# Performance work log

Measured on AMD Instinct MI355X. Metric: run time of the kernel, lower is better.

## Reference

```python
import jax, jax.numpy as jnp
import numpy as np
import math

# Model dims (match init_kwargs)
N = 2048      # columns
DS = 64       # d_state
DI = 256      # d_input
DV = 64       # d_vote
K = 512       # k_active = int(N * 0.25)
H = 4         # bus attention heads
HD = DV // H  # head dim
MULT = 4
B, T = 2, 4


def _rmsnorm(x, w, eps=1e-6):
    return w * x * jax.lax.rsqrt(jnp.mean(x * x, axis=-1, keepdims=True) + eps)


def setup_inputs() -> dict:
    key = jax.random.key(0)
    ks = jax.random.split(key, 12)
    s = 0.02
    dcat = DS + DS + DV  # concat[h, x, m]
    return {
        "x": jax.random.normal(ks[0], (B, T, DI), jnp.float32),
        "W_in": jax.random.normal(ks[1], (DS, DI), jnp.float32) * s,
        "core_norm_w": jnp.ones((dcat,), jnp.float32),
        "core_Wg": jax.random.normal(ks[2], (2 * MULT * DS, dcat), jnp.float32) * s,
        "core_Wout": jax.random.normal(ks[3], (DS, MULT * DS), jnp.float32) * s,
        "W_gate": jax.random.normal(ks[4], (1, DS), jnp.float32) * s,
        "W_vote": jax.random.normal(ks[5], (DV, DS), jnp.float32) * s,
        "attn_in_w": jax.random.normal(ks[6], (3 * DV, DV), jnp.float32) * s,
        "attn_out_w": jax.random.normal(ks[7], (DV, DV), jnp.float32) * s,
        "W_film_scale": jax.random.normal(ks[8], (DS, DV), jnp.float32) * s,
        "W_film_shift": jax.random.normal(ks[9], (DS, DV), jnp.float32) * s,
        "query": jax.random.normal(ks[10], (1, 1, DS), jnp.float32),
        "out_norm_w": jnp.ones((DS,), jnp.float32),
        "W_out": jax.random.normal(ks[11], (DI, DS), jnp.float32) * s,
    }


def _forward(x, W_in, core_norm_w, core_Wg, core_Wout, W_gate, W_vote,
             attn_in_w, attn_out_w, W_film_scale, W_film_shift, query,
             out_norm_w, W_out):
    Bsz = x.shape[0]
    Wq, Wk, Wv = jnp.split(attn_in_w, 3, axis=0)
    bidx = jnp.arange(Bsz)[:, None]

    def step(h, x_t):
        # input projection, broadcast to every column
        x_proj = x_t @ W_in.T                                     # (B, DS)
        x_rep = jnp.broadcast_to(x_proj[:, None, :], (Bsz, N, DS))
        # top-k gating with straight-through soft scores
        gate = jnp.squeeze(h @ W_gate.T, -1)                      # (B, N)
        _, idx = jax.lax.top_k(gate, K)
        mask_hard = jnp.zeros((Bsz, N), x.dtype).at[bidx, idx].set(1.0)
        mask_soft = jax.nn.softmax(gate, axis=-1)
        ms = (mask_hard + mask_soft - jax.lax.stop_gradient(mask_soft))[..., None]
        # column core: RMSNorm -> SwiGLU -> proj -> residual (m = zeros)
        z = _rmsnorm(jnp.concatenate(
            [h, x_rep, jnp.zeros((Bsz, N, DV), x.dtype)], axis=-1), core_norm_w)
        a, b = jnp.split(z @ core_Wg.T, 2, axis=-1)
        h_hat = h + (a * jax.nn.silu(b)) @ core_Wout.T
        h = h + ms * (h_hat - h)
        # votes, masked to active columns
        v = (h @ W_vote.T) * ms                                   # (B, N, DV)
        # bus self-attention with key padding mask on inactive columns
        qh = (v @ Wq.T).reshape(Bsz, N, H, HD)
        kh = (v @ Wk.T).reshape(Bsz, N, H, HD)
        vh = (v @ Wv.T).reshape(Bsz, N, H, HD)
        logits = jnp.einsum('bqhd,bkhd->bhqk', qh, kh) / math.sqrt(HD)
        pad = mask_hard == 0.0
        logits = jnp.where(pad[:, None, None, :], -jnp.inf, logits)
        attnw = jax.nn.softmax(logits, axis=-1)
        m = jnp.einsum('bhqk,bkhd->bqhd', attnw, vh).reshape(Bsz, N, DV) @ attn_out_w.T
        # FiLM modulation
        h = h * (1.0 + jnp.tanh(m @ W_film_scale.T)) + m @ W_film_shift.T
        # learned-query pooling over columns
        pl = jnp.einsum('d,bnd->bn', query[0, 0], h) / math.sqrt(DS)
        pw = jax.nn.softmax(pl, axis=-1)
        pooled = jnp.einsum('bn,bnd->bd', pw, h)
        y = _rmsnorm(pooled, out_norm_w) @ W_out.T               # (B, DI)
        return h, y

    h0 = jnp.zeros((Bsz, N, DS), x.dtype)  # fresh state per forward (reset_state)
    _, ys = jax.lax.scan(step, h0, jnp.swapaxes(x, 0, 1))
    return jnp.swapaxes(ys, 0, 1)  # (B, T, DI)


def reference(x, W_in, core_norm_w, core_Wg, core_Wout, W_gate, W_vote,
              attn_in_w, attn_out_w, W_film_scale, W_film_shift, query,
              out_norm_w, W_out):
    return _forward(x, W_in, core_norm_w, core_Wg, core_Wout, W_gate, W_vote,
                    attn_in_w, attn_out_w, W_film_scale, W_film_shift, query,
                    out_norm_w, W_out)
```

## Files before the change

kernel.cpp:

```cpp
#include <hip/hip_runtime.h>
#include <hip/hip_bf16.h>

#define NN 2048
#define DS 64
#define DI 256
#define DV 64
#define KK 512
#define HH 4
#define HD 16
#define BB 2
#define TT 4
#define DCAT 192

typedef unsigned long long ull;

__device__ __forceinline__ float wave_sum(float v) {
#pragma unroll
    for (int o = 32; o > 0; o >>= 1) v += __shfl_xor(v, o);
    return v;
}
__device__ __forceinline__ float wave_max(float v) {
#pragma unroll
    for (int o = 32; o > 0; o >>= 1) v = fmaxf(v, __shfl_xor(v, o));
    return v;
}
__device__ __forceinline__ unsigned enc_f(float f) {
    unsigned u = __float_as_uint(f);
    return (u & 0x80000000u) ? ~u : (u | 0x80000000u);
}

__global__ __launch_bounds__(256) void k_pre(
    const float* __restrict__ x, const float* __restrict__ W_in,
    const float* __restrict__ attn_in_w, const float* __restrict__ W_vote,
    const float* __restrict__ attn_out_w, const float* __restrict__ Wfs,
    const float* __restrict__ Wfsh,
    float* __restrict__ xproj, int* __restrict__ col2slot, int* __restrict__ act_idx,
    float* __restrict__ Wqkv, float* __restrict__ Wsc, float* __restrict__ Wsh)
{
    int blk = blockIdx.x, tid = threadIdx.x;
    int w = tid >> 6, lane = tid & 63;
    if (blk < 8) {
        int b = blk >> 2, t = blk & 3;
        int r = tid >> 2, q = tid & 3;
        const float* xp = x + (b * TT + t) * DI + q * 64;
        const float* wr = W_in + r * DI + q * 64;
        float a = 0.f;
#pragma unroll
        for (int i = 0; i < 64; i++) a += xp[i] * wr[i];
        a += __shfl_xor(a, 1); a += __shfl_xor(a, 2);
        if (q == 0) xproj[(b * TT + t) * DS + r] = a;
    } else if (blk < 10) {
        int b = blk - 8;
        for (int i = tid; i < NN; i += 256) col2slot[b * NN + i] = (i < KK) ? i : -1;
        for (int i = tid; i < KK; i += 256) act_idx[b * KK + i] = i;
    } else if (blk < 58) {
        int r = (blk - 10) * 4 + w;
        const float* ar = attn_in_w + r * 64;
        float acc = 0.f;
#pragma unroll
        for (int e = 0; e < 64; e++) acc += ar[e] * W_vote[e * 64 + lane];
        Wqkv[r * 64 + lane] = acc;
    } else if (blk < 74) {
        int r = (blk - 58) * 4 + w;
        const float* ar = Wfs + r * 64;
        float acc = 0.f;
#pragma unroll
        for (int e = 0; e < 64; e++) acc += ar[e] * attn_out_w[e * 64 + lane];
        Wsc[r * 64 + lane] = acc;
    } else {
        int r = (blk - 74) * 4 + w;
        const float* ar = Wfsh + r * 64;
        float acc = 0.f;
#pragma unroll
        for (int e = 0; e < 64; e++) acc += ar[e] * attn_out_w[e * 64 + lane];
        Wsh[r * 64 + lane] = acc;
    }
}

__global__ __launch_bounds__(256) void k_head(
    const float* __restrict__ gate, int* __restrict__ col2slot,
    int* __restrict__ act_idx,
    const float* __restrict__ ppool, const float* __restrict__ psum,
    const float* __restrict__ pmax, const float* __restrict__ onw,
    const float* __restrict__ W_out, float* __restrict__ out, int t)
{
    __shared__ char sm[20480];
    __shared__ ull s_prefix; __shared__ int s_need; __shared__ unsigned ccnt;
    __shared__ float pn[64];
    int blk = blockIdx.x, tid = threadIdx.x;
    int w = tid >> 6, lane = tid & 63;
    if (blk < 2) {
        if (t >= TT) return;
        int b = blk;
        ull* keys = (ull*)sm;
        unsigned (*hist4)[256] = (unsigned(*)[256])(sm + 16384);
        if (tid == 0) ccnt = 0;
        for (int i = tid; i < NN; i += 256) {
            keys[i] = ((ull)enc_f(gate[b * NN + i]) << 11) | (unsigned)(NN - 1 - i);
            col2slot[b * NN + i] = -1;
        }
        ull prefix = 0, pmask = 0;
        int need = KK;
        for (int shift = 40; shift >= 0; shift -= 8) {
            for (int k = lane; k < 256; k += 64) hist4[w][k] = 0;
            __syncthreads();
            for (int i = tid; i < NN; i += 256) {
                ull k = keys[i];
                if ((k & pmask) == prefix)
                    atomicAdd(&hist4[w][(unsigned)((k >> shift) & 255)], 1u);
            }
            __syncthreads();
            if (w == 0) {
                unsigned c0 = hist4[0][4 * lane]     + hist4[1][4 * lane]     + hist4[2][4 * lane]     + hist4[3][4 * lane];
                unsigned c1 = hist4[0][4 * lane + 1] + hist4[1][4 * lane + 1] + hist4[2][4 * lane + 1] + hist4[3][4 * lane + 1];
                unsigned c2 = hist4[0][4 * lane + 2] + hist4[1][4 * lane + 2] + hist4[2][4 * lane + 2] + hist4[3][4 * lane + 2];
                unsigned c3 = hist4[0][4 * lane + 3] + hist4[1][4 * lane + 3] + hist4[2][4 * lane + 3] + hist4[3][4 * lane + 3];
                unsigned s3 = c3, s2 = c2 + s3, s1 = c1 + s2, s0 = c0 + s1;
                unsigned run = s0;
#pragma unroll
                for (int off = 1; off < 64; off <<= 1) {
                    unsigned v = __shfl_down(run, off);
                    if (lane + off < 64) run += v;
                }
                unsigned higher = run - s0;
                unsigned suf0 = s0 + higher, suf1 = s1 + higher, suf2 = s2 + higher, suf3 = s3 + higher;
                unsigned nd = (unsigned)need;
                if (suf0 >= nd && suf1 < nd) { s_prefix = prefix | ((ull)(4 * lane)     << shift); s_need = need - (int)suf1; }
                if (suf1 >= nd && suf2 < nd) { s_prefix = prefix | ((ull)(4 * lane + 1) << shift); s_need = need - (int)suf2; }
                if (suf2 >= nd && suf3 < nd) { s_prefix = prefix | ((ull)(4 * lane + 2) << shift); s_need = need - (int)suf3; }
                if (suf3 >= nd && higher < nd) { s_prefix = prefix | ((ull)(4 * lane + 3) << shift); s_need = need - (int)higher; }
            }
            __syncthreads();
            prefix = s_prefix; need = s_need; pmask |= (0xFFull << shift);
        }
        for (int i = tid; i < NN; i += 256) {
            ull k = keys[i];
            if (k >= prefix) {
                unsigned p = atomicAdd(&ccnt, 1u);
                int n = NN - 1 - (int)(k & 2047ull);
                act_idx[b * KK + p] = n;
                col2slot[b * NN + n] = (int)p;
            }
        }
    } else {
        if (t == 0) return;
        int b = blk - 2;
        if (tid < 64) {
            int d = tid;
            float gm = -1e30f;
            for (int i = 0; i < 64; i++) gm = fmaxf(gm, pmax[b * 64 + i]);
            float s = 0.f, v = 0.f;
            for (int i = 0; i < 64; i++) {
                float e = __expf(pmax[b * 64 + i] - gm);
                s += psum[b * 64 + i] * e;
                v += ppool[(b * 64 + i) * 64 + d] * e;
            }
            float val = v / s;
            float ss = wave_sum(val * val);
            float rs = rsqrtf(ss * (1.0f / DS) + 1e-6f);
            pn[d] = onw[d] * val * rs;
        }
        __syncthreads();
        {
            int o = tid;
            const float* wr = W_out + o * DS;
            float a = 0.f;
#pragma unroll
            for (int d = 0; d < DS; d++) a += pn[d] * wr[d];
            out[(b * TT + (t - 1)) * DI + o] = a;
        }
    }
}

__global__ __launch_bounds__(256) void k_core_a(
    const float* __restrict__ h, const float* __restrict__ xproj,
    const int* __restrict__ act_idx, const float* __restrict__ norm_w,
    const float* __restrict__ Wg, const float* __restrict__ Wout,
    float* __restrict__ part16, int t)
{
    __shared__ char sm[34048];
    int tid = threadIdx.x;
    int cg = blockIdx.x >> 4;
    int og = blockIdx.x & 15;
    int c = tid & 63;
    int seg = __builtin_amdgcn_readfirstlane(tid >> 6);
    int b = cg >> 3;
    int sbase = (cg & 7) * 64;
    float* zt  = (float*)sm;
    float* ssq = (float*)(sm + 32768);
    float* rsb = (float*)(sm + 33792);
    {
        int n = act_idx[b * KK + sbase + c];
        float vals[32];
        float sq = 0.f;
        if (seg < 2) {
            const float* hp = h + ((size_t)(b * NN + n)) * DS + seg * 32;
#pragma unroll
            for (int i = 0; i < 32; i++) { float v = hp[i]; vals[i] = v; sq += v * v; }
        } else {
            const float* xp = xproj + (b * TT + t) * DS + (seg - 2) * 32;
#pragma unroll
            for (int i = 0; i < 32; i++) { float v = xp[i]; vals[i] = v; sq += v * v; }
        }
        ssq[seg * 64 + c] = sq;
        __syncthreads();
        if (tid < 64) {
            float s = ssq[tid] + ssq[64 + tid] + ssq[128 + tid] + ssq[192 + tid];
            rsb[tid] = rsqrtf(s * (1.0f / DCAT) + 1e-6f);
        }
        __syncthreads();
        {
            float rs = rsb[c];
#pragma unroll
            for (int i = 0; i < 32; i++) {
                int d = seg * 32 + i;
                zt[d * 64 + c] = norm_w[d] * vals[i] * rs;
            }
        }
    }
    __syncthreads();
    float z[128];
#pragma unroll
    for (int d = 0; d < 128; d++) z[d] = zt[d * 64 + c];
    __syncthreads();
    float* u16  = (float*)sm;
    float* tile = (float*)(sm + 4096);
    int rbase = og * 16 + seg * 4;
    float ga[4];
#pragma unroll
    for (int r = 0; r < 4; r++) {
        const float* wr = Wg + (rbase + r) * DCAT;
        float acc = 0.f;
#pragma unroll
        for (int d = 0; d < 128; d++) acc += z[d] * wr[d];
        ga[r] = acc;
    }
#pragma unroll
    for (int r = 0; r < 4; r++) {
        const float* wr = Wg + (256 + rbase + r) * DCAT;
        float bacc = 0.f;
#pragma unroll
        for (int d = 0; d < 128; d++) bacc += z[d] * wr[d];
        float uu = ga[r] * (bacc / (1.f + expf(-bacc)));
        u16[(seg * 4 + r) * 64 + c] = uu;
    }
    __syncthreads();
    {
        int w = tid >> 6;
#pragma unroll
        for (int oi = 0; oi < 16; oi++) {
            int o = w * 16 + oi;
            const float* wr = Wout + o * 256 + og * 16;
            float acc = 0.f;
#pragma unroll
            for (int r = 0; r < 16; r++) acc += u16[r * 64 + c] * wr[r];
            tile[o * 65 + c] = acc;
        }
    }
    __syncthreads();
    {
        int gcolbase = cg * 64;
#pragma unroll
        for (int k = 0; k < 16; k++) {
            int flat = k * 256 + tid;
            int gl = flat >> 6, oo = flat & 63;
            part16[(size_t)(gcolbase + gl) * 1024 + og * 64 + oo] = tile[oo * 65 + gl];
        }
    }
}

__global__ __launch_bounds__(256) void k_vqkv(
    float* __restrict__ h, const float* __restrict__ part16,
    const int* __restrict__ act_idx, const float* __restrict__ Wqkv,
    float* __restrict__ qh, float* __restrict__ kh, float* __restrict__ vh)
{
    __shared__ float hn[64 * 33];
    __shared__ int an[32];
    int blk = blockIdx.x;
    int b = blk >> 4;
    int sbase = (blk & 15) * 32;
    int tid = threadIdx.x;
    int w = __builtin_amdgcn_readfirstlane(tid >> 6);
    int l = tid & 63;
    int c = l & 31, sub = l >> 5;
    if (tid < 32) an[tid] = act_idx[b * KK + sbase + tid];
    __syncthreads();
    {
        int o = tid & 63;
#pragma unroll
        for (int k = 0; k < 8; k++) {
            int s = (tid >> 6) + k * 4;
            const float* pp = part16 + (size_t)(b * KK + sbase + s) * 1024 + o;
            float sum = 0.f;
#pragma unroll
            for (int kk = 0; kk < 16; kk++) sum += pp[kk * 64];
            size_t hidx = ((size_t)(b * NN + an[s])) * DS + o;
            float nh = h[hidx] + sum;
            h[hidx] = nh;
            hn[o * 33 + s] = nh;
        }
    }
    __syncthreads();
    float hh[32];
#pragma unroll
    for (int i = 0; i < 32; i++) hh[i] = hn[(sub * 32 + i) * 33 + c];
    int slot = sbase + c;
#pragma unroll 4
    for (int oi = 0; oi < 48; oi++) {
        int r = w * 48 + oi;
        const float* wr = Wqkv + r * 64 + sub * 32;
        float a = 0.f;
#pragma unroll
        for (int i = 0; i < 32; i++) a += hh[i] * wr[i];
        a += __shfl_xor(a, 32);
        if (sub == 0) {
            if (r < 64) {
                qh[((b * HH + (r >> 4)) * HD + (r & 15)) * KK + slot] = a;
            } else if (r < 128) {
                int rr = r - 64;
                kh[((b * HH + (rr >> 4)) * HD + (rr & 15)) * KK + slot] = a;
            } else {
                int rr = r - 128;
                vh[((b * HH + (rr >> 4)) * HD + (rr & 15)) * KK + slot] = a;
            }
        }
    }
}

__global__ __launch_bounds__(256) void k_attn(
    const float* __restrict__ qh, const float* __restrict__ kh,
    const float* __restrict__ vh, float* __restrict__ m_raw,
    const float* __restrict__ Wsc, const float* __restrict__ Wsh,
    float* __restrict__ fsm, float* __restrict__ fshm)
{
    __shared__ float partm[4 * 64];
    __shared__ float mr[64];
    int blk = blockIdx.x;
    int tid = threadIdx.x;
    if (blk < 2) {
        int b = blk;
        int w = tid >> 6, lane = tid & 63;
        float macc[64];
#pragma unroll
        for (int d = 0; d < 64; d++) macc[d] = 0.f;
        for (int s = tid; s < KK; s += 256) {
#pragma unroll
            for (int d = 0; d < 64; d++) macc[d] += vh[(b * DV + d) * KK + s];
        }
#pragma unroll
        for (int d = 0; d < 64; d++) macc[d] = wave_sum(macc[d]);
        if (lane == 0) {
#pragma unroll
            for (int d = 0; d < 64; d++) partm[w * 64 + d] = macc[d];
        }
        __syncthreads();
        if (tid < 64)
            mr[tid] = (partm[tid] + partm[64 + tid] + partm[128 + tid] + partm[192 + tid]) * (1.0f / KK);
        __syncthreads();
        if (tid < 64) {
            const float* ws_ = Wsc + tid * DV;
            const float* wh_ = Wsh + tid * DV;
            float sc = 0.f, sh = 0.f;
#pragma unroll
            for (int e = 0; e < 64; e++) { float zz = mr[e]; sc += ws_[e] * zz; sh += wh_[e] * zz; }
            fsm[b * DS + tid] = tanhf(sc);
            fshm[b * DS + tid] = sh;
        }
        return;
    }
    int wave = tid >> 6, lane = tid & 63;
    int task = (blk - 2) * 4 + wave;
    int qs = task & (KK - 1);
    int bh = task >> 9;
    float q[HD];
#pragma unroll
    for (int d = 0; d < HD; d++) q[d] = qh[(bh * HD + d) * KK + qs];
    const float* kp = kh + bh * HD * KK;
    const float* vp = vh + bh * HD * KK;
    float lg[8]; float mx = -1e30f;
#pragma unroll
    for (int i = 0; i < 8; i++) {
        int slot = i * 64 + lane;
        float a = 0.f;
#pragma unroll
        for (int d = 0; d < HD; d++) a += q[d] * kp[d * KK + slot];
        lg[i] = a * 0.25f;
        mx = fmaxf(mx, lg[i]);
    }
    mx = wave_max(mx);
    float p[8]; float sum = 0.f;
#pragma unroll
    for (int i = 0; i < 8; i++) { p[i] = __expf(lg[i] - mx); sum += p[i]; }
    sum = wave_sum(sum);
    float inv = 1.0f / sum;
    float acc[HD];
#pragma unroll
    for (int d = 0; d < HD; d++) acc[d] = 0.f;
#pragma unroll
    for (int i = 0; i < 8; i++) {
        int slot = i * 64 + lane;
        float pi = p[i];
#pragma unroll
        for (int d = 0; d < HD; d++) acc[d] += pi * vp[d * KK + slot];
    }
#pragma unroll
    for (int d = 0; d < HD; d++) acc[d] = wave_sum(acc[d]) * inv;
    if (lane == 0) {
        int b = bh >> 2, head = bh & 3;
#pragma unroll
        for (int d = 0; d < HD; d++)
            m_raw[(b * DV + head * HD + d) * KK + qs] = acc[d];
    }
}

__global__ __launch_bounds__(256) void k_pool3(
    float* __restrict__ h, const int* __restrict__ col2slot,
    const float* __restrict__ fsm, const float* __restrict__ fshm,
    const float* __restrict__ m_raw, const float* __restrict__ Wsc,
    const float* __restrict__ Wsh, const float* __restrict__ query,
    const float* __restrict__ W_gate, float* __restrict__ gate,
    float* __restrict__ ppool, float* __restrict__ psum, float* __restrict__ pmax)
{
    __shared__ int slots[32];
    __shared__ float M[64 * 33];
    __shared__ float SCT[32 * 65];
    __shared__ float SHT[32 * 65];
    __shared__ float wvecs[4][64];
    __shared__ float wms[4], wss[4];
    int blk = blockIdx.x;
    int b = blk >> 6;
    int base = (blk & 63) * 32;
    int tid = threadIdx.x;
    int w = tid >> 6, lane = tid & 63;
    if (tid < 32) slots[tid] = col2slot[b * NN + base + tid];
    __syncthreads();
    for (int idx = tid; idx < 2048; idx += 256) {
        int d = idx >> 5, c = idx & 31;
        int s = slots[c];
        M[d * 33 + c] = (s >= 0) ? m_raw[(b * DV + d) * KK + s] : 0.f;
    }
    __syncthreads();
    {
        int sc_col = lane & 31, half = lane >> 5;
        int act = slots[sc_col] >= 0;
#pragma unroll 4
        for (int oi = 0; oi < 16; oi++) {
            int o = w * 16 + oi;
            const float* ws_ = Wsc + o * DV + half * 32;
            const float* wh_ = Wsh + o * DV + half * 32;
            float sc = 0.f, sh = 0.f;
#pragma unroll
            for (int e = 0; e < 32; e++) {
                float zz = M[(half * 32 + e) * 33 + sc_col];
                sc += ws_[e] * zz; sh += wh_[e] * zz;
            }
            sc += __shfl_xor(sc, 32); sh += __shfl_xor(sh, 32);
            if (half == 0) {
                SCT[sc_col * 65 + o] = act ? tanhf(sc) : fsm[b * DS + o];
                SHT[sc_col * 65 + o] = act ? sh : fshm[b * DS + o];
            }
        }
    }
    __syncthreads();
    float qv = query[lane] * 0.125f, wg = W_gate[lane];
    float wm = -1e30f, sw = 0.f, vec = 0.f;
#pragma unroll
    for (int ci = 0; ci < 8; ci++) {
        int cl = w * 8 + ci;
        int n = base + cl;
        size_t idx = ((size_t)(b * NN + n)) * DS + lane;
        float hv = h[idx];
        hv = hv * (1.f + SCT[cl * 65 + lane]) + SHT[cl * 65 + lane];
        h[idx] = hv;
        float lg = wave_sum(qv * hv);
        float gt = wave_sum(wg * hv);
        if (lane == 0) gate[b * NN + n] = gt;
        float nm = fmaxf(wm, lg);
        float scale = __expf(wm - nm);
        float e = __expf(lg - nm);
        sw = sw * scale + e;
        vec = vec * scale + e * hv;
        wm = nm;
    }
    wvecs[w][lane] = vec;
    if (lane == 0) { wms[w] = wm; wss[w] = sw; }
    __syncthreads();
    if (tid < 64) {
        float m4 = fmaxf(fmaxf(wms[0], wms[1]), fmaxf(wms[2], wms[3]));
        float s = 0.f, v = 0.f;
#pragma unroll
        for (int ww = 0; ww < 4; ww++) {
            float e = __expf(wms[ww] - m4);
            s += wss[ww] * e;
            v += wvecs[ww][tid] * e;
        }
        ppool[blk * 64 + tid] = v;
        if (tid == 0) { psum[blk] = s; pmax[blk] = m4; }
    }
}

extern "C" void kernel_launch(void* const* d_in, const int* in_sizes, int n_in,
                              void* d_out, int out_size, void* d_ws, size_t ws_size,
                              hipStream_t stream)
{
    const float* x          = (const float*)d_in[0];
    const float* W_in       = (const float*)d_in[1];
    const float* core_norm_w= (const float*)d_in[2];
    const float* core_Wg    = (const float*)d_in[3];
    const float* core_Wout  = (const float*)d_in[4];
    const float* W_gate     = (const float*)d_in[5];
    const float* W_vote     = (const float*)d_in[6];
    const float* attn_in_w  = (const float*)d_in[7];
    const float* attn_out_w = (const float*)d_in[8];
    const float* Wfs        = (const float*)d_in[9];
    const float* Wfsh       = (const float*)d_in[10];
    const float* query      = (const float*)d_in[11];
    const float* onw        = (const float*)d_in[12];
    const float* W_out      = (const float*)d_in[13];
    float* out = (float*)d_out;

    float* ws = (float*)d_ws;
    float* h        = ws;
    float* gate     = h + (size_t)BB * NN * DS;
    float* xproj    = gate + BB * NN;
    int*   col2slot = (int*)(xproj + BB * TT * DS);
    int*   act_idx  = col2slot + BB * NN;
    float* part16   = (float*)(act_idx + BB * KK);
    float* qh       = part16 + 1024 * 1024;
    float* kh       = qh + BB * HH * KK * HD;
    float* vh       = kh + BB * HH * KK * HD;
    float* m_raw    = vh + BB * HH * KK * HD;
    float* fsm      = m_raw + BB * DV * KK;
    float* fshm     = fsm + BB * DS;
    float* ppool    = fshm + BB * DS;
    float* psum     = ppool + 128 * 64;
    float* pmax     = psum + 128;
    float* Wqkv     = pmax + 128;
    float* Wsc      = Wqkv + 192 * 64;
    float* Wsh      = Wsc + 64 * 64;

    hipMemsetAsync(h, 0, (size_t)BB * NN * DS * sizeof(float), stream);

    k_pre<<<90, 256, 0, stream>>>(x, W_in, attn_in_w, W_vote, attn_out_w, Wfs, Wfsh,
                                  xproj, col2slot, act_idx, Wqkv, Wsc, Wsh);
    for (int t = 0; t < TT; t++) {
        if (t > 0)
            k_head<<<4, 256, 0, stream>>>(gate, col2slot, act_idx, ppool, psum, pmax,
                                          onw, W_out, out, t);
        k_core_a<<<256, 256, 0, stream>>>(h, xproj, act_idx, core_norm_w, core_Wg,
                                          core_Wout, part16, t);
        k_vqkv<<<32, 256, 0, stream>>>(h, part16, act_idx, Wqkv, qh, kh, vh);
        k_attn<<<1026, 256, 0, stream>>>(qh, kh, vh, m_raw, Wsc, Wsh, fsm, fshm);
        k_pool3<<<128, 256, 0, stream>>>(h, col2slot, fsm, fshm, m_raw, Wsc, Wsh,
                                         query, W_gate, gate, ppool, psum, pmax);
    }
    k_head<<<4, 256, 0, stream>>>(gate, col2slot, act_idx, ppool, psum, pmax,
                                  onw, W_out, out, TT);
}
```

Before: 358.2 us.

## Fuse head kernel into pool kernel via last-block atomic completion counter

```diff
diff --git a/kernel.cpp b/kernel.cpp
--- a/kernel.cpp
+++ b/kernel.cpp
@@ -74,101 +74,6 @@
 #pragma unroll
         for (int e = 0; e < 64; e++) acc += ar[e] * attn_out_w[e * 64 + lane];
         Wsh[r * 64 + lane] = acc;
-    }
-}
-
-__global__ __launch_bounds__(256) void k_head(
-    const float* __restrict__ gate, int* __restrict__ col2slot,
-    int* __restrict__ act_idx,
-    const float* __restrict__ ppool, const float* __restrict__ psum,
-    const float* __restrict__ pmax, const float* __restrict__ onw,
-    const float* __restrict__ W_out, float* __restrict__ out, int t)
-{
-    __shared__ char sm[20480];
-    __shared__ ull s_prefix; __shared__ int s_need; __shared__ unsigned ccnt;
-    __shared__ float pn[64];
-    int blk = blockIdx.x, tid = threadIdx.x;
-    int w = tid >> 6, lane = tid & 63;
-    if (blk < 2) {
-        if (t >= TT) return;
-        int b = blk;
-        ull* keys = (ull*)sm;
-        unsigned (*hist4)[256] = (unsigned(*)[256])(sm + 16384);
-        if (tid == 0) ccnt = 0;
-        for (int i = tid; i < NN; i += 256) {
-            keys[i] = ((ull)enc_f(gate[b * NN + i]) << 11) | (unsigned)(NN - 1 - i);
-            col2slot[b * NN + i] = -1;
-        }
-        ull prefix = 0, pmask = 0;
-        int need = KK;
-        for (int shift = 40; shift >= 0; shift -= 8) {
-            for (int k = lane; k < 256; k += 64) hist4[w][k] = 0;
-            __syncthreads();
-            for (int i = tid; i < NN; i += 256) {
-                ull k = keys[i];
-                if ((k & pmask) == prefix)
-                    atomicAdd(&hist4[w][(unsigned)((k >> shift) & 255)], 1u);
-            }
-            __syncthreads();
-            if (w == 0) {
-                unsigned c0 = hist4[0][4 * lane]     + hist4[1][4 * lane]     + hist4[2][4 * lane]     + hist4[3][4 * lane];
-                unsigned c1 = hist4[0][4 * lane + 1] + hist4[1][4 * lane + 1] + hist4[2][4 * lane + 1] + hist4[3][4 * lane + 1];
-                unsigned c2 = hist4[0][4 * lane + 2] + hist4[1][4 * lane + 2] + hist4[2][4 * lane + 2] + hist4[3][4 * lane + 2];
-                unsigned c3 = hist4[0][4 * lane + 3] + hist4[1][4 * lane + 3] + hist4[2][4 * lane + 3] + hist4[3][4 * lane + 3];
-                unsigned s3 = c3, s2 = c2 + s3, s1 = c1 + s2, s0 = c0 + s1;
-                unsigned run = s0;
-#pragma unroll
-                for (int off = 1; off < 64; off <<= 1) {
-                    unsigned v = __shfl_down(run, off);
-                    if (lane + off < 64) run += v;
-                }
-                unsigned higher = run - s0;
-                unsigned suf0 = s0 + higher, suf1 = s1 + higher, suf2 = s2 + higher, suf3 = s3 + higher;
-                unsigned nd = (unsigned)need;
-                if (suf0 >= nd && suf1 < nd) { s_prefix = prefix | ((ull)(4 * lane)     << shift); s_need = need - (int)suf1; }
-                if (suf1 >= nd && suf2 < nd) { s_prefix = prefix | ((ull)(4 * lane + 1) << shift); s_need = need - (int)suf2; }
-                if (suf2 >= nd && suf3 < nd) { s_prefix = prefix | ((ull)(4 * lane + 2) << shift); s_need = need - (int)suf3; }
-                if (suf3 >= nd && higher < nd) { s_prefix = prefix | ((ull)(4 * lane + 3) << shift); s_need = need - (int)higher; }
-            }
-            __syncthreads();
-            prefix = s_prefix; need = s_need; pmask |= (0xFFull << shift);
-        }
-        for (int i = tid; i < NN; i += 256) {
-            ull k = keys[i];
-            if (k >= prefix) {
-                unsigned p = atomicAdd(&ccnt, 1u);
-                int n = NN - 1 - (int)(k & 2047ull);
-                act_idx[b * KK + p] = n;
-                col2slot[b * NN + n] = (int)p;
-            }
-        }
-    } else {
-        if (t == 0) return;
-        int b = blk - 2;
-        if (tid < 64) {
-            int d = tid;
-            float gm = -1e30f;
-            for (int i = 0; i < 64; i++) gm = fmaxf(gm, pmax[b * 64 + i]);
-            float s = 0.f, v = 0.f;
-            for (int i = 0; i < 64; i++) {
-                float e = __expf(pmax[b * 64 + i] - gm);
-                s += psum[b * 64 + i] * e;
-                v += ppool[(b * 64 + i) * 64 + d] * e;
-            }
-            float val = v / s;
-            float ss = wave_sum(val * val);
-            float rs = rsqrtf(ss * (1.0f / DS) + 1e-6f);
-            pn[d] = onw[d] * val * rs;
-        }
-        __syncthreads();
-        {
-            int o = tid;
-            const float* wr = W_out + o * DS;
-            float a = 0.f;
-#pragma unroll
-            for (int d = 0; d < DS; d++) a += pn[d] * wr[d];
-            out[(b * TT + (t - 1)) * DI + o] = a;
-        }
     }
 }
 
@@ -414,19 +319,25 @@
 }
 
 __global__ __launch_bounds__(256) void k_pool3(
-    float* __restrict__ h, const int* __restrict__ col2slot,
+    float* __restrict__ h, int* __restrict__ col2slot,
     const float* __restrict__ fsm, const float* __restrict__ fshm,
     const float* __restrict__ m_raw, const float* __restrict__ Wsc,
     const float* __restrict__ Wsh, const float* __restrict__ query,
     const float* __restrict__ W_gate, float* __restrict__ gate,
-    float* __restrict__ ppool, float* __restrict__ psum, float* __restrict__ pmax)
+    float* __restrict__ ppool, float* __restrict__ psum, float* __restrict__ pmax,
+    unsigned* __restrict__ done, const float* __restrict__ onw,
+    const float* __restrict__ W_out, float* __restrict__ out,
+    int* __restrict__ act_idx, int t)
 {
-    __shared__ int slots[32];
-    __shared__ float M[64 * 33];
-    __shared__ float SCT[32 * 65];
-    __shared__ float SHT[32 * 65];
-    __shared__ float wvecs[4][64];
+    __shared__ char smem[26368];
     __shared__ float wms[4], wss[4];
+    __shared__ int lastsh;
+    __shared__ ull s_prefix; __shared__ int s_need; __shared__ unsigned ccnt;
+    int* slots  = (int*)smem;
+    float* M    = (float*)(smem + 128);
+    float* SCT  = (float*)(smem + 8576);
+    float* SHT  = (float*)(smem + 16896);
+    float* wvecs= (float*)(smem + 25216);
     int blk = blockIdx.x;
     int b = blk >> 6;
     int base = (blk & 63) * 32;
@@ -462,28 +373,30 @@
         }
     }
     __syncthreads();
-    float qv = query[lane] * 0.125f, wg = W_gate[lane];
-    float wm = -1e30f, sw = 0.f, vec = 0.f;
-#pragma unroll
-    for (int ci = 0; ci < 8; ci++) {
-        int cl = w * 8 + ci;
-        int n = base + cl;
-        size_t idx = ((size_t)(b * NN + n)) * DS + lane;
-        float hv = h[idx];
-        hv = hv * (1.f + SCT[cl * 65 + lane]) + SHT[cl * 65 + lane];
-        h[idx] = hv;
-        float lg = wave_sum(qv * hv);
-        float gt = wave_sum(wg * hv);
-        if (lane == 0) gate[b * NN + n] = gt;
-        float nm = fmaxf(wm, lg);
-        float scale = __expf(wm - nm);
-        float e = __expf(lg - nm);
-        sw = sw * scale + e;
-        vec = vec * scale + e * hv;
-        wm = nm;
-    }
-    wvecs[w][lane] = vec;
-    if (lane == 0) { wms[w] = wm; wss[w] = sw; }
+    {
+        float qv = query[lane] * 0.125f, wg = W_gate[lane];
+        float wm = -1e30f, sw = 0.f, vec = 0.f;
+#pragma unroll
+        for (int ci = 0; ci < 8; ci++) {
+            int cl = w * 8 + ci;
+            int n = base + cl;
+            size_t idx = ((size_t)(b * NN + n)) * DS + lane;
+            float hv = h[idx];
+            hv = hv * (1.f + SCT[cl * 65 + lane]) + SHT[cl * 65 + lane];
+            h[idx] = hv;
+            float lg = wave_sum(qv * hv);
+            float gt = wave_sum(wg * hv);
+            if (lane == 0) gate[b * NN + n] = gt;
+            float nm = fmaxf(wm, lg);
+            float scale = __expf(wm - nm);
+            float e = __expf(lg - nm);
+            sw = sw * scale + e;
+            vec = vec * scale + e * hv;
+            wm = nm;
+        }
+        wvecs[w * 64 + lane] = vec;
+        if (lane == 0) { wms[w] = wm; wss[w] = sw; }
+    }
     __syncthreads();
     if (tid < 64) {
         float m4 = fmaxf(fmaxf(wms[0], wms[1]), fmaxf(wms[2], wms[3]));
@@ -492,10 +405,95 @@
         for (int ww = 0; ww < 4; ww++) {
             float e = __expf(wms[ww] - m4);
             s += wss[ww] * e;
-            v += wvecs[ww][tid] * e;
+            v += wvecs[ww * 64 + tid] * e;
         }
         ppool[blk * 64 + tid] = v;
         if (tid == 0) { psum[blk] = s; pmax[blk] = m4; }
+    }
+    __syncthreads();
+    if (tid == 0) {
+        unsigned old = __hip_atomic_fetch_add(&done[t * BB + b], 1u,
+                                              __ATOMIC_ACQ_REL, __HIP_MEMORY_SCOPE_AGENT);
+        lastsh = (old == 63);
+    }
+    __syncthreads();
+    if (!lastsh) return;
+    float* pn = (float*)(smem + 20480);
+    if (tid < 64) {
+        int d = tid;
+        float gm = -1e30f;
+        for (int i = 0; i < 64; i++) gm = fmaxf(gm, pmax[b * 64 + i]);
+        float s = 0.f, v = 0.f;
+        for (int i = 0; i < 64; i++) {
+            float e = __expf(pmax[b * 64 + i] - gm);
+            s += psum[b * 64 + i] * e;
+            v += ppool[(b * 64 + i) * 64 + d] * e;
+        }
+        float val = v / s;
+        float ss = wave_sum(val * val);
+        float rs = rsqrtf(ss * (1.0f / DS) + 1e-6f);
+        pn[d] = onw[d] * val * rs;
+    }
+    __syncthreads();
+    {
+        int o = tid;
+        const float* wr = W_out + o * DS;
+        float a = 0.f;
+#pragma unroll
+        for (int d = 0; d < DS; d++) a += pn[d] * wr[d];
+        out[(b * TT + t) * DI + o] = a;
+    }
+    if (t == TT - 1) return;
+    ull* keys = (ull*)smem;
+    unsigned (*hist4)[256] = (unsigned(*)[256])(smem + 16384);
+    __syncthreads();
+    if (tid == 0) ccnt = 0;
+    for (int i = tid; i < NN; i += 256) {
+        keys[i] = ((ull)enc_f(gate[b * NN + i]) << 11) | (unsigned)(NN - 1 - i);
+        col2slot[b * NN + i] = -1;
+    }
+    ull prefix = 0, pmask = 0;
+    int need = KK;
+    for (int shift = 40; shift >= 0; shift -= 8) {
+        for (int k = lane; k < 256; k += 64) hist4[w][k] = 0;
+        __syncthreads();
+        for (int i = tid; i < NN; i += 256) {
+            ull k = keys[i];
+            if ((k & pmask) == prefix)
+                atomicAdd(&hist4[w][(unsigned)((k >> shift) & 255)], 1u);
+        }
+        __syncthreads();
+        if (w == 0) {
+            unsigned c0 = hist4[0][4 * lane]     + hist4[1][4 * lane]     + hist4[2][4 * lane]     + hist4[3][4 * lane];
+            unsigned c1 = hist4[0][4 * lane + 1] + hist4[1][4 * lane + 1] + hist4[2][4 * lane + 1] + hist4[3][4 * lane + 1];
+            unsigned c2 = hist4[0][4 * lane + 2] + hist4[1][4 * lane + 2] + hist4[2][4 * lane + 2] + hist4[3][4 * lane + 2];
+            unsigned c3 = hist4[0][4 * lane + 3] + hist4[1][4 * lane + 3] + hist4[2][4 * lane + 3] + hist4[3][4 * lane + 3];
+            unsigned s3 = c3, s2 = c2 + s3, s1 = c1 + s2, s0 = c0 + s1;
+            unsigned run = s0;
+#pragma unroll
+            for (int off = 1; off < 64; off <<= 1) {
+                unsigned v = __shfl_down(run, off);
+                if (lane + off < 64) run += v;
+            }
+            unsigned higher = run - s0;
+            unsigned suf0 = s0 + higher, suf1 = s1 + higher, suf2 = s2 + higher, suf3 = s3 + higher;
+            unsigned nd = (unsigned)need;
+            if (suf0 >= nd && suf1 < nd) { s_prefix = prefix | ((ull)(4 * lane)     << shift); s_need = need - (int)suf1; }
+            if (suf1 >= nd && suf2 < nd) { s_prefix = prefix | ((ull)(4 * lane + 1) << shift); s_need = need - (int)suf2; }
+            if (suf2 >= nd && suf3 < nd) { s_prefix = prefix | ((ull)(4 * lane + 2) << shift); s_need = need - (int)suf3; }
+            if (suf3 >= nd && higher < nd) { s_prefix = prefix | ((ull)(4 * lane + 3) << shift); s_need = need - (int)higher; }
+        }
+        __syncthreads();
+        prefix = s_prefix; need = s_need; pmask |= (0xFFull << shift);
+    }
+    for (int i = tid; i < NN; i += 256) {
+        ull k = keys[i];
+        if (k >= prefix) {
+            unsigned p = atomicAdd(&ccnt, 1u);
+            int n = NN - 1 - (int)(k & 2047ull);
+            act_idx[b * KK + p] = n;
+            col2slot[b * NN + n] = (int)p;
+        }
     }
 }
 
@@ -521,7 +519,8 @@
 
     float* ws = (float*)d_ws;
     float* h        = ws;
-    float* gate     = h + (size_t)BB * NN * DS;
+    unsigned* done  = (unsigned*)(h + (size_t)BB * NN * DS);
+    float* gate     = (float*)(done + 16);
     float* xproj    = gate + BB * NN;
     int*   col2slot = (int*)(xproj + BB * TT * DS);
     int*   act_idx  = col2slot + BB * NN;
@@ -539,21 +538,17 @@
     float* Wsc      = Wqkv + 192 * 64;
     float* Wsh      = Wsc + 64 * 64;
 
-    hipMemsetAsync(h, 0, (size_t)BB * NN * DS * sizeof(float), stream);
+    hipMemsetAsync(h, 0, (size_t)BB * NN * DS * sizeof(float) + 64, stream);
 
     k_pre<<<90, 256, 0, stream>>>(x, W_in, attn_in_w, W_vote, attn_out_w, Wfs, Wfsh,
                                   xproj, col2slot, act_idx, Wqkv, Wsc, Wsh);
     for (int t = 0; t < TT; t++) {
-        if (t > 0)
-            k_head<<<4, 256, 0, stream>>>(gate, col2slot, act_idx, ppool, psum, pmax,
-                                          onw, W_out, out, t);
         k_core_a<<<256, 256, 0, stream>>>(h, xproj, act_idx, core_norm_w, core_Wg,
                                           core_Wout, part16, t);
         k_vqkv<<<32, 256, 0, stream>>>(h, part16, act_idx, Wqkv, qh, kh, vh);
         k_attn<<<1026, 256, 0, stream>>>(qh, kh, vh, m_raw, Wsc, Wsh, fsm, fshm);
         k_pool3<<<128, 256, 0, stream>>>(h, col2slot, fsm, fshm, m_raw, Wsc, Wsh,
-                                         query, W_gate, gate, ppool, psum, pmax);
-    }
-    k_head<<<4, 256, 0, stream>>>(gate, col2slot, act_idx, ppool, psum, pmax,
-                                  onw, W_out, out, TT);
-}
+                                         query, W_gate, gate, ppool, psum, pmax,
+                                         done, onw, W_out, out, act_idx, t);
+    }
+}
```

Result: slower. 411.6 us (+14.9%).
